# Performance work log

Hardware: AMD Instinct MI355X
Metric: run time of the kernel (lower is better)

## Reference

```python
import jax, jax.numpy as jnp
import numpy as np

B, N, D = 8, 2048, 256

def setup_inputs() -> dict:
    key = jax.random.key(0)
    ks = jax.random.split(key, 8)
    sc = 1.0 / np.sqrt(D)
    return {
        "x": jax.random.normal(ks[0], (B, N, D), dtype=jnp.float32),
        "W_fp": jax.random.normal(ks[1], (D, D), dtype=jnp.float32) * sc,
        "b_fp": jnp.zeros((D,), dtype=jnp.float32),
        "w_s": jax.random.normal(ks[2], (D,), dtype=jnp.float32) * sc,
        "b_s": jnp.zeros((), dtype=jnp.float32),
        "W_rp": jax.random.normal(ks[3], (D, D), dtype=jnp.float32) * sc,
        "b_rp": jnp.zeros((D,), dtype=jnp.float32),
        "W_gp": jax.random.normal(ks[4], (D, D), dtype=jnp.float32) * sc,
        "b_gp": jnp.zeros((D,), dtype=jnp.float32),
        "gamma": jnp.ones((D,), dtype=jnp.float32),
        "beta": jnp.zeros((D,), dtype=jnp.float32),
    }

def reference(x, W_fp, b_fp, w_s, b_s, W_rp, b_rp, W_gp, b_gp, gamma, beta):
    # feature projection: [B, N, D]
    proj = jnp.einsum('bnd,de->bne', x, W_fp) + b_fp
    # F.normalize(p=2, dim=-1) with eps=1e-12
    nrm = jnp.sqrt(jnp.sum(proj * proj, axis=-1, keepdims=True))
    xn = proj / jnp.maximum(nrm, 1e-12)
    # cosine similarity matrix [B, N, N]
    sim = jnp.einsum('bnd,bmd->bnm', xn, xn)
    # adj_scaler: Linear(D,1)+sigmoid is constant along the broadcast axis ->
    # compute per-node scalar once [B, N] (same math as the O(N^2*D) expand)
    s = jax.nn.sigmoid(jnp.einsum('bnd,d->bn', proj, w_s) + b_s)
    scaler = jnp.clip(0.5 * (s[:, :, None] + s[:, None, :]), 1e-6, 1.0)
    adj = jnp.maximum(scaler * sim, 1e-6)  # clamp(min=1e-6)
    degree = jnp.maximum(jnp.sum(adj, axis=2, keepdims=True), 1e-6)
    norm_adj = adj / degree
    # aggregation + region projection
    region = jnp.einsum('bnm,bmd->bnd', norm_adj, proj)
    region = jnp.einsum('bnd,de->bne', region, W_rp) + b_rp
    # global pooling + projection: [B, 1, D]
    g = jnp.mean(region, axis=1, keepdims=True)
    g = jnp.einsum('bnd,de->bne', g, W_gp) + b_gp
    input_global = jnp.mean(x, axis=1, keepdims=True)
    h = g + input_global
    # LayerNorm (eps=1e-5)
    mu = jnp.mean(h, axis=-1, keepdims=True)
    var = jnp.mean((h - mu) ** 2, axis=-1, keepdims=True)
    out = (h - mu) / jnp.sqrt(var + 1e-5) * gamma + beta
    return out, adj
```

## Files before the change

kernel.cpp:

```cpp
#include <hip/hip_runtime.h>
#include <hip/hip_bf16.h>
#include <math.h>

#define Bn 8
#define Nn 2048
#define Dn 256

typedef short short8 __attribute__((ext_vector_type(8)));
typedef float floatx4 __attribute__((ext_vector_type(4)));

__device__ __forceinline__ short f2bf_bits(float f) {
    __bf16 h = (__bf16)f;
    return __builtin_bit_cast(short, h);
}

__device__ __forceinline__ float bf2f(short s) {
    unsigned u = ((unsigned)(unsigned short)s) << 16;
    return __builtin_bit_cast(float, u);
}

__device__ __forceinline__ void gl_lds16(const void* gsrc, void* ldst) {
    __builtin_amdgcn_global_load_lds(
        (const __attribute__((address_space(1))) void*)gsrc,
        (__attribute__((address_space(3))) void*)ldst, 16, 0, 0);
}

__device__ __forceinline__ float sigmoidf_(float z) {
    return 1.0f / (1.0f + __expf(-z));
}



__global__ __launch_bounds__(256) void k_transpose(const float* __restrict__ W,
                                                   short* __restrict__ Wt) {
    __shared__ float Ts[64][65];
    const int t = threadIdx.x;
    const int dt0 = blockIdx.x * 64, et0 = blockIdx.y * 64;
    const int ro = t >> 4, co = (t & 15) * 4;
    #pragma unroll
    for (int rr = 0; rr < 4; ++rr) {
        int row = rr * 16 + ro;
        float4 v = *(const float4*)(W + (size_t)(dt0 + row) * Dn + et0 + co);
        Ts[row][co + 0] = v.x; Ts[row][co + 1] = v.y;
        Ts[row][co + 2] = v.z; Ts[row][co + 3] = v.w;
    }
    __syncthreads();
    const int e = t >> 2, cd0 = (t & 3) * 16;
    short8 a, b;
    #pragma unroll
    for (int i = 0; i < 8; ++i) {
        a[i] = f2bf_bits(Ts[cd0 + i][e]);
        b[i] = f2bf_bits(Ts[cd0 + 8 + i][e]);
    }
    *(short8*)(Wt + (size_t)(et0 + e) * Dn + dt0 + cd0) = a;
    *(short8*)(Wt + (size_t)(et0 + e) * Dn + dt0 + cd0 + 8) = b;
}


__global__ __launch_bounds__(512) void k_projxn(
    const float* __restrict__ x, const short* __restrict__ Wt,
    const float* __restrict__ b_fp, const float* __restrict__ w_s,
    short* __restrict__ xn, float* __restrict__ sdot, float* __restrict__ nrm,
    float* __restrict__ xpart) {
    __shared__ __align__(16) short As[64 * 64];
    __shared__ __align__(16) short Bs[256 * 64];
    __shared__ float xsumS[8 * 256];
    __shared__ float redW[2][64];
    __shared__ float redN[2][64];
    const int t = threadIdx.x;
    const int bm = blockIdx.x * 64;
    const int lane = t & 63, wv = t >> 6;
    const int wm = (wv & 3) * 16;
    const int jh = wv >> 2;
    const int l15 = lane & 15, q = lane >> 4;
    const int rx = l15 & 7;

    for (int i = t; i < 2048; i += 512) xsumS[i] = 0.f;

    floatx4 acc[8];
    #pragma unroll
    for (int j = 0; j < 8; ++j) acc[j] = (floatx4){0.f, 0.f, 0.f, 0.f};

    const int rA = t >> 3, cA = (t & 7) * 8;
    const int rB = t >> 3;
    const int swzA = ((t & 7) ^ (rA & 7)) * 8;
    const int swzBsrc = ((t & 7) ^ (rB & 7)) * 8;
    const int cB = (t & 7) * 8;

    for (int k0 = 0; k0 < Dn; k0 += 64) {
        const float* gp = x + (size_t)(bm + rA) * Dn + k0 + cA;
        float4 v0 = *(const float4*)gp;
        float4 v1 = *(const float4*)(gp + 4);
        short8 o0;
        o0[0] = f2bf_bits(v0.x); o0[1] = f2bf_bits(v0.y);
        o0[2] = f2bf_bits(v0.z); o0[3] = f2bf_bits(v0.w);
        o0[4] = f2bf_bits(v1.x); o0[5] = f2bf_bits(v1.y);
        o0[6] = f2bf_bits(v1.z); o0[7] = f2bf_bits(v1.w);
        *(short8*)(As + rA * 64 + swzA) = o0;
        #pragma unroll
        for (int cc = 0; cc < 4; ++cc)
            gl_lds16(Wt + (size_t)(cc * 64 + rB) * Dn + k0 + swzBsrc,
                     Bs + (cc * 64 + rB) * 64 + cB);
        __syncthreads();
        #pragma unroll
        for (int ks = 0; ks < 2; ++ks) {
            const int cs = ((ks * 4 + q) ^ rx) * 8;
            short8 af = *(const short8*)(As + (wm + l15) * 64 + cs);
            #pragma unroll
            for (int jj = 0; jj < 8; ++jj) {
                short8 bfr = *(const short8*)(Bs + (jh * 128 + jj * 16 + l15) * 64 + cs);
                acc[jj] = __builtin_amdgcn_mfma_f32_16x16x32_bf16(af, bfr, acc[jj], 0, 0, 0);
            }
        }
        {
            float s = 0.f;
            #pragma unroll
            for (int r = 0; r < 8; ++r) {
                int row = wv * 8 + r;
                int idx = ((lane >> 3) ^ (row & 7)) * 8 + (lane & 7);
                s += bf2f(As[row * 64 + idx]);
            }
            xsumS[wv * 256 + k0 + lane] += s;
        }
        __syncthreads();
    }
    if (t < 256) {
        float xs = 0.f;
        #pragma unroll
        for (int w = 0; w < 8; ++w) xs += xsumS[w * 256 + t];
        xpart[(size_t)blockIdx.x * Dn + t] = xs;
    }
    float bfv[8], wsv[8];
    #pragma unroll
    for (int jj = 0; jj < 8; ++jj) {
        bfv[jj] = b_fp[jh * 128 + jj * 16 + l15];
        wsv[jj] = w_s[jh * 128 + jj * 16 + l15];
    }
    float vv[4][8];
    #pragma unroll
    for (int reg = 0; reg < 4; ++reg) {
        float pw = 0.f, pn = 0.f;
        #pragma unroll
        for (int jj = 0; jj < 8; ++jj) {
            float v = acc[jj][reg] + bfv[jj];
            vv[reg][jj] = v;
            pw += v * wsv[jj];
            pn += v * v;
        }
        #pragma unroll
        for (int m = 1; m < 16; m <<= 1) {
            pw += __shfl_xor(pw, m);
            pn += __shfl_xor(pn, m);
        }
        if (l15 == 0) {
            redW[jh][wm + q * 4 + reg] = pw;
            redN[jh][wm + q * 4 + reg] = pn;
        }
    }
    __syncthreads();
    #pragma unroll
    for (int reg = 0; reg < 4; ++reg) {
        int lr = wm + q * 4 + reg;
        float pw = redW[0][lr] + redW[1][lr];
        float pn = redN[0][lr] + redN[1][lr];
        float nc = fmaxf(sqrtf(pn), 1e-12f);
        float inv = 1.0f / nc;
        int row = bm + lr;
        size_t rbase = (size_t)row * Dn + jh * 128 + l15;
        #pragma unroll
        for (int jj = 0; jj < 8; ++jj)
            xn[rbase + jj * 16] = f2bf_bits(vv[reg][jj] * inv);
        if (jh == 0 && l15 == 0) {
            sdot[row] = pw;
            nrm[row] = nc;
        }
    }
}


__global__ __launch_bounds__(512) void k_sim(
    const short* __restrict__ xn, const float* __restrict__ sdot,
    const float* __restrict__ b_s, float* __restrict__ adj,
    float* __restrict__ deg_part) {
    __shared__ __align__(16) short As[128 * 64];
    __shared__ __align__(16) short Bs[256 * 64];
    __shared__ float degS[4][128];
    const int t = threadIdx.x;
    int lin = (blockIdx.z * 16 + blockIdx.y) * 8 + blockIdx.x;
    const int b = lin & 7;
    const int pos = lin >> 3;
    const int by = pos >> 3, cx = pos & 7;
    const int bm = by * 128;
    const int bn = cx * 256;
    const int lane = t & 63, wv = t >> 6;
    const int wm = (wv >> 2) * 64;
    const int wn = (wv & 3) * 64;
    const int l15 = lane & 15, q4 = lane >> 4;
    const int rx = l15 & 7;
    const int rr = t >> 3, c8 = (t & 7) * 8;
    const int swzSrc = ((t & 7) ^ (rr & 7)) * 8;
    const short* xb = xn + (size_t)b * Nn * Dn;

    floatx4 acc[4][4];
    #pragma unroll
    for (int i = 0; i < 4; ++i)
        #pragma unroll
        for (int j = 0; j < 4; ++j) acc[i][j] = (floatx4){0.f, 0.f, 0.f, 0.f};

    for (int k0 = 0; k0 < Dn; k0 += 64) {
        #pragma unroll
        for (int cc = 0; cc < 2; ++cc) {
            int r = cc * 64 + rr;
            gl_lds16(xb + (size_t)(bm + r) * Dn + k0 + swzSrc, As + r * 64 + c8);
        }
        #pragma unroll
        for (int cc = 0; cc < 4; ++cc) {
            int r = cc * 64 + rr;
            gl_lds16(xb + (size_t)(bn + r) * Dn + k0 + swzSrc, Bs + r * 64 + c8);
        }
        __syncthreads();
        #pragma unroll
        for (int ks = 0; ks < 2; ++ks) {
            const int cs = ((ks * 4 + q4) ^ rx) * 8;
            short8 af[4], bfr[4];
            #pragma unroll
            for (int i = 0; i < 4; ++i)
                af[i] = *(const short8*)(As + (wm + i * 16 + l15) * 64 + cs);
            #pragma unroll
            for (int j = 0; j < 4; ++j)
                bfr[j] = *(const short8*)(Bs + (wn + j * 16 + l15) * 64 + cs);
            #pragma unroll
            for (int i = 0; i < 4; ++i)
                #pragma unroll
                for (int j = 0; j < 4; ++j)
                    acc[i][j] = __builtin_amdgcn_mfma_f32_16x16x32_bf16(bfr[j], af[i], acc[i][j], 0, 0, 0);
        }
        __syncthreads();
    }
    const float bsv = b_s[0];
    float srow[4];
    #pragma unroll
    for (int i = 0; i < 4; ++i)
        srow[i] = sigmoidf_(sdot[b * Nn + bm + wm + i * 16 + l15] + bsv);
    float scol[4][4];
    #pragma unroll
    for (int j = 0; j < 4; ++j)
        #pragma unroll
        for (int reg = 0; reg < 4; ++reg)
            scol[j][reg] = sigmoidf_(sdot[b * Nn + bn + wn + j * 16 + q4 * 4 + reg] + bsv);
    #pragma unroll
    for (int i = 0; i < 4; ++i) {
        float rs = 0.f;
        size_t rbase = ((size_t)b * Nn + (bm + wm + i * 16 + l15)) * Nn + bn + wn + q4 * 4;
        #pragma unroll
        for (int j = 0; j < 4; ++j) {
            float4 o;
            float sc;
            sc = fminf(fmaxf(0.5f * (srow[i] + scol[j][0]), 1e-6f), 1.0f);
            o.x = fmaxf(sc * acc[i][j][0], 1e-6f);
            sc = fminf(fmaxf(0.5f * (srow[i] + scol[j][1]), 1e-6f), 1.0f);
            o.y = fmaxf(sc * acc[i][j][1], 1e-6f);
            sc = fminf(fmaxf(0.5f * (srow[i] + scol[j][2]), 1e-6f), 1.0f);
            o.z = fmaxf(sc * acc[i][j][2], 1e-6f);
            sc = fminf(fmaxf(0.5f * (srow[i] + scol[j][3]), 1e-6f), 1.0f);
            o.w = fmaxf(sc * acc[i][j][3], 1e-6f);
            *(float4*)(adj + rbase + (size_t)j * 16) = o;
            rs += o.x + o.y + o.z + o.w;
        }
        rs += __shfl_xor(rs, 16);
        rs += __shfl_xor(rs, 32);
        if (q4 == 0) degS[wv & 3][wm + i * 16 + l15] = rs;
    }
    __syncthreads();
    if (t < 128)
        deg_part[((size_t)(b * 8 + cx)) * Nn + bm + t] =
            degS[0][t] + degS[1][t] + degS[2][t] + degS[3][t];
}


__global__ __launch_bounds__(256) void k_deg(const float* __restrict__ deg_part,
                                             float* __restrict__ invdeg) {
    int b = blockIdx.x, t = blockIdx.y * 256 + threadIdx.x;
    float s = 0.f;
    #pragma unroll
    for (int cx = 0; cx < 8; ++cx)
        s += deg_part[((size_t)(b * 8 + cx)) * Nn + t];
    invdeg[b * Nn + t] = 1.0f / fmaxf(s, 1e-6f);
}


__global__ __launch_bounds__(1024) void k_colsum(
    const float* __restrict__ adj, const float* __restrict__ invdeg,
    const short* __restrict__ xn, const float* __restrict__ nrm,
    float* __restrict__ gpart) {
    int b = blockIdx.x, ck = blockIdx.y, t = threadIdx.x;
    __shared__ float invS[Nn];
    __shared__ float part[64][64];
    __shared__ float csL[64];
    __shared__ float gQ[4][Dn];
    invS[t] = invdeg[b * Nn + t];
    invS[t + 1024] = invdeg[b * Nn + t + 1024];
    __syncthreads();
    const int lc = (t & 15) * 4;
    const int rg = t >> 4;
    const int c0 = ck * 64;
    float sx = 0.f, sy = 0.f, sz = 0.f, sw = 0.f;
    for (int r = rg; r < Nn; r += 64) {
        float4 v = *(const float4*)(adj + ((size_t)b * Nn + r) * Nn + c0 + lc);
        float w = invS[r];
        sx += v.x * w; sy += v.y * w; sz += v.z * w; sw += v.w * w;
    }
    part[rg][lc + 0] = sx; part[rg][lc + 1] = sy;
    part[rg][lc + 2] = sz; part[rg][lc + 3] = sw;
    __syncthreads();
    if (t < 64) {
        float s = 0.f;
        #pragma unroll
        for (int g = 0; g < 64; ++g) s += part[g][t];
        csL[t] = s * nrm[b * Nn + c0 + t];
    }
    __syncthreads();
    {
        int h = t >> 8, d = t & 255;
        float g = 0.f;
        #pragma unroll 4
        for (int mi = 0; mi < 16; ++mi) {
            int m = h * 16 + mi;
            g += csL[m] * bf2f(xn[((size_t)(b * Nn + c0 + m)) * Dn + d]);
        }
        gQ[h][d] = g;
    }
    __syncthreads();
    if (t < Dn)
        gpart[(b * 32 + ck) * Dn + t] = gQ[0][t] + gQ[1][t] + gQ[2][t] + gQ[3][t];
}


__global__ __launch_bounds__(1024) void k_final2(
    const float* __restrict__ gpart, const float* __restrict__ xpart,
    const float* __restrict__ W_rp, const float* __restrict__ b_rp,
    const float* __restrict__ W_gp, const float* __restrict__ b_gp,
    const float* __restrict__ gamma, const float* __restrict__ beta,
    float* __restrict__ out) {
    int b = blockIdx.x, t = threadIdx.x;
    const int d = t & 255, c4 = t >> 8;
    __shared__ float pS[4][Dn];
    __shared__ float xS[4][Dn];
    __shared__ float gp_s[Dn];
    __shared__ float xm_s[Dn];
    __shared__ float g1_s[Dn];
    __shared__ float red[8];
    {
        float gs = 0.f, xs = 0.f;
        #pragma unroll
        for (int k = 0; k < 8; ++k) {
            int ck = c4 * 8 + k;
            gs += gpart[(b * 32 + ck) * Dn + d];
            xs += xpart[(b * 32 + ck) * Dn + d];
        }
        pS[c4][d] = gs;
        xS[c4][d] = xs;
    }
    __syncthreads();
    if (t < Dn) {
        gp_s[t] = (pS[0][t] + pS[1][t] + pS[2][t] + pS[3][t]) * (1.0f / Nn);
        xm_s[t] = (xS[0][t] + xS[1][t] + xS[2][t] + xS[3][t]) * (1.0f / Nn);
    }
    __syncthreads();
    {
        float m1 = 0.f;
        #pragma unroll 4
        for (int i = 0; i < 64; ++i) {
            int dd = c4 * 64 + i;
            m1 += gp_s[dd] * W_rp[dd * Dn + d];
        }
        pS[c4][d] = m1;
    }
    __syncthreads();
    if (t < Dn) g1_s[t] = b_rp[t] + pS[0][t] + pS[1][t] + pS[2][t] + pS[3][t];
    __syncthreads();
    {
        float m2 = 0.f;
        #pragma unroll 4
        for (int i = 0; i < 64; ++i) {
            int ee = c4 * 64 + i;
            m2 += g1_s[ee] * W_gp[ee * Dn + d];
        }
        pS[c4][d] = m2;
    }
    __syncthreads();
    float h = 0.f;
    if (t < Dn) {
        h = b_gp[t] + pS[0][t] + pS[1][t] + pS[2][t] + pS[3][t] + xm_s[t];
        float sum = h;
        #pragma unroll
        for (int m = 1; m < 64; m <<= 1) sum += __shfl_xor(sum, m);
        if ((t & 63) == 0) red[t >> 6] = sum;
    }
    __syncthreads();
    float mu = (red[0] + red[1] + red[2] + red[3]) * (1.0f / Dn);
    if (t < Dn) {
        float dv = h - mu;
        float s2 = dv * dv;
        #pragma unroll
        for (int m = 1; m < 64; m <<= 1) s2 += __shfl_xor(s2, m);
        if ((t & 63) == 0) red[4 + (t >> 6)] = s2;
    }
    __syncthreads();
    if (t < Dn) {
        float dv = h - mu;
        float var = (red[4] + red[5] + red[6] + red[7]) * (1.0f / Dn);
        out[b * Dn + t] = dv * rsqrtf(var + 1e-5f) * gamma[t] + beta[t];
    }
}


extern "C" void kernel_launch(void* const* d_in, const int* in_sizes, int n_in,
                              void* d_out, int out_size, void* d_ws, size_t ws_size,
                              hipStream_t stream) {
    const float* x     = (const float*)d_in[0];
    const float* W_fp  = (const float*)d_in[1];
    const float* b_fp  = (const float*)d_in[2];
    const float* w_s   = (const float*)d_in[3];
    const float* b_s   = (const float*)d_in[4];
    const float* W_rp  = (const float*)d_in[5];
    const float* b_rp  = (const float*)d_in[6];
    const float* W_gp  = (const float*)d_in[7];
    const float* b_gp  = (const float*)d_in[8];
    const float* gamma = (const float*)d_in[9];
    const float* beta  = (const float*)d_in[10];

    float* out = (float*)d_out;
    float* adj = out + Bn * Dn;

    char* ws = (char*)d_ws;
    short* xn     = (short*)(ws);
    short* Wt     = (short*)(ws + 8388608);
    float* sdot   = (float*)(ws + 8519680);
    float* nrm    = (float*)(ws + 8585216);
    float* degp   = (float*)(ws + 8650752);
    float* invdeg = (float*)(ws + 9175040);
    float* gpart  = (float*)(ws + 9699328);
    float* xpart  = (float*)(ws + 9961472);

    k_transpose<<<dim3(4, 4), 256, 0, stream>>>(W_fp, Wt);
    k_projxn<<<(Bn * Nn) / 64, 512, 0, stream>>>(x, Wt, b_fp, w_s, xn, sdot, nrm, xpart);
    k_sim<<<dim3(8, 16, 8), 512, 0, stream>>>(xn, sdot, b_s, adj, degp);
    k_deg<<<dim3(Bn, 8), 256, 0, stream>>>(degp, invdeg);
    k_colsum<<<dim3(Bn, 32), 1024, 0, stream>>>(adj, invdeg, xn, nrm, gpart);
    k_final2<<<Bn, 1024, 0, stream>>>(gpart, xpart, W_rp, b_rp, W_gp, b_gp, gamma, beta, out);
}
```

Before: 237.9 us.

## Fuse degree reduction and final projection into colsum via last-block atomic counter

The separate k_deg kernel is removed: each colsum block now sums the eight degree partials for its batch and computes inverse degrees itself. The k_final2 kernel is folded into k_colsum using a per-batch atomic counter, so the last block to finish a batch runs the pooled projections and LayerNorm. Counters are zeroed in k_transpose. This cuts two kernel launches and their gaps, at the cost of redundant degree reduction in every block (32x per batch) and a serialized tail on the last block.

```diff
diff --git a/kernel.cpp b/kernel.cpp
--- a/kernel.cpp
+++ b/kernel.cpp
@@ -30,11 +30,12 @@
 }
 
 
-
 __global__ __launch_bounds__(256) void k_transpose(const float* __restrict__ W,
-                                                   short* __restrict__ Wt) {
+                                                   short* __restrict__ Wt,
+                                                   unsigned* __restrict__ cnt) {
     __shared__ float Ts[64][65];
     const int t = threadIdx.x;
+    if (blockIdx.x == 0 && blockIdx.y == 0 && t < 8) cnt[t] = 0u;
     const int dt0 = blockIdx.x * 64, et0 = blockIdx.y * 64;
     const int ro = t >> 4, co = (t & 15) * 4;
     #pragma unroll
@@ -278,28 +279,29 @@
 }
 
 
-__global__ __launch_bounds__(256) void k_deg(const float* __restrict__ deg_part,
-                                             float* __restrict__ invdeg) {
-    int b = blockIdx.x, t = blockIdx.y * 256 + threadIdx.x;
-    float s = 0.f;
-    #pragma unroll
-    for (int cx = 0; cx < 8; ++cx)
-        s += deg_part[((size_t)(b * 8 + cx)) * Nn + t];
-    invdeg[b * Nn + t] = 1.0f / fmaxf(s, 1e-6f);
-}
-
-
 __global__ __launch_bounds__(1024) void k_colsum(
-    const float* __restrict__ adj, const float* __restrict__ invdeg,
+    const float* __restrict__ adj, const float* __restrict__ deg_part,
     const short* __restrict__ xn, const float* __restrict__ nrm,
-    float* __restrict__ gpart) {
+    float* __restrict__ gpart, const float* __restrict__ xpart,
+    const float* __restrict__ W_rp, const float* __restrict__ b_rp,
+    const float* __restrict__ W_gp, const float* __restrict__ b_gp,
+    const float* __restrict__ gamma, const float* __restrict__ beta,
+    float* __restrict__ out, unsigned* __restrict__ cnt) {
     int b = blockIdx.x, ck = blockIdx.y, t = threadIdx.x;
     __shared__ float invS[Nn];
     __shared__ float part[64][64];
     __shared__ float csL[64];
     __shared__ float gQ[4][Dn];
-    invS[t] = invdeg[b * Nn + t];
-    invS[t + 1024] = invdeg[b * Nn + t + 1024];
+    __shared__ int doneFlag;
+    #pragma unroll
+    for (int rc = 0; rc < 2; ++rc) {
+        int row = rc * 1024 + t;
+        float s = 0.f;
+        #pragma unroll
+        for (int cx = 0; cx < 8; ++cx)
+            s += deg_part[((size_t)(b * 8 + cx)) * Nn + row];
+        invS[row] = 1.0f / fmaxf(s, 1e-6f);
+    }
     __syncthreads();
     const int lc = (t & 15) * 4;
     const int rg = t >> 4;
@@ -333,84 +335,85 @@
     __syncthreads();
     if (t < Dn)
         gpart[(b * 32 + ck) * Dn + t] = gQ[0][t] + gQ[1][t] + gQ[2][t] + gQ[3][t];
-}
-
-
-__global__ __launch_bounds__(1024) void k_final2(
-    const float* __restrict__ gpart, const float* __restrict__ xpart,
-    const float* __restrict__ W_rp, const float* __restrict__ b_rp,
-    const float* __restrict__ W_gp, const float* __restrict__ b_gp,
-    const float* __restrict__ gamma, const float* __restrict__ beta,
-    float* __restrict__ out) {
-    int b = blockIdx.x, t = threadIdx.x;
-    const int d = t & 255, c4 = t >> 8;
-    __shared__ float pS[4][Dn];
-    __shared__ float xS[4][Dn];
-    __shared__ float gp_s[Dn];
-    __shared__ float xm_s[Dn];
-    __shared__ float g1_s[Dn];
-    __shared__ float red[8];
+    __syncthreads();
+    if (t == 0) {
+        __threadfence();
+        unsigned old = atomicAdd(&cnt[b], 1u);
+        doneFlag = (old == 31u);
+    }
+    __syncthreads();
+    if (!doneFlag) return;
+    __threadfence();
     {
-        float gs = 0.f, xs = 0.f;
-        #pragma unroll
-        for (int k = 0; k < 8; ++k) {
-            int ck = c4 * 8 + k;
-            gs += gpart[(b * 32 + ck) * Dn + d];
-            xs += xpart[(b * 32 + ck) * Dn + d];
-        }
-        pS[c4][d] = gs;
-        xS[c4][d] = xs;
-    }
-    __syncthreads();
-    if (t < Dn) {
-        gp_s[t] = (pS[0][t] + pS[1][t] + pS[2][t] + pS[3][t]) * (1.0f / Nn);
-        xm_s[t] = (xS[0][t] + xS[1][t] + xS[2][t] + xS[3][t]) * (1.0f / Nn);
-    }
-    __syncthreads();
-    {
-        float m1 = 0.f;
-        #pragma unroll 4
-        for (int i = 0; i < 64; ++i) {
-            int dd = c4 * 64 + i;
-            m1 += gp_s[dd] * W_rp[dd * Dn + d];
-        }
-        pS[c4][d] = m1;
-    }
-    __syncthreads();
-    if (t < Dn) g1_s[t] = b_rp[t] + pS[0][t] + pS[1][t] + pS[2][t] + pS[3][t];
-    __syncthreads();
-    {
-        float m2 = 0.f;
-        #pragma unroll 4
-        for (int i = 0; i < 64; ++i) {
-            int ee = c4 * 64 + i;
-            m2 += g1_s[ee] * W_gp[ee * Dn + d];
-        }
-        pS[c4][d] = m2;
-    }
-    __syncthreads();
-    float h = 0.f;
-    if (t < Dn) {
-        h = b_gp[t] + pS[0][t] + pS[1][t] + pS[2][t] + pS[3][t] + xm_s[t];
-        float sum = h;
-        #pragma unroll
-        for (int m = 1; m < 64; m <<= 1) sum += __shfl_xor(sum, m);
-        if ((t & 63) == 0) red[t >> 6] = sum;
-    }
-    __syncthreads();
-    float mu = (red[0] + red[1] + red[2] + red[3]) * (1.0f / Dn);
-    if (t < Dn) {
-        float dv = h - mu;
-        float s2 = dv * dv;
-        #pragma unroll
-        for (int m = 1; m < 64; m <<= 1) s2 += __shfl_xor(s2, m);
-        if ((t & 63) == 0) red[4 + (t >> 6)] = s2;
-    }
-    __syncthreads();
-    if (t < Dn) {
-        float dv = h - mu;
-        float var = (red[4] + red[5] + red[6] + red[7]) * (1.0f / Dn);
-        out[b * Dn + t] = dv * rsqrtf(var + 1e-5f) * gamma[t] + beta[t];
+        const int d = t & 255, c4 = t >> 8;
+        float (*pS)[Dn] = (float(*)[Dn])&part[0][0];
+        float (*xS)[Dn] = (float(*)[Dn])&part[16][0];
+        float* gp_s = &part[32][0];
+        float* xm_s = &part[36][0];
+        float* g1_s = &part[40][0];
+        float* red  = &part[44][0];
+        {
+            float gs = 0.f, xs = 0.f;
+            #pragma unroll
+            for (int k = 0; k < 8; ++k) {
+                int kk = c4 * 8 + k;
+                gs += gpart[(b * 32 + kk) * Dn + d];
+                xs += xpart[(b * 32 + kk) * Dn + d];
+            }
+            pS[c4][d] = gs;
+            xS[c4][d] = xs;
+        }
+        __syncthreads();
+        if (t < Dn) {
+            gp_s[t] = (pS[0][t] + pS[1][t] + pS[2][t] + pS[3][t]) * (1.0f / Nn);
+            xm_s[t] = (xS[0][t] + xS[1][t] + xS[2][t] + xS[3][t]) * (1.0f / Nn);
+        }
+        __syncthreads();
+        {
+            float m1 = 0.f;
+            #pragma unroll 4
+            for (int i = 0; i < 64; ++i) {
+                int dd = c4 * 64 + i;
+                m1 += gp_s[dd] * W_rp[dd * Dn + d];
+            }
+            pS[c4][d] = m1;
+        }
+        __syncthreads();
+        if (t < Dn) g1_s[t] = b_rp[t] + pS[0][t] + pS[1][t] + pS[2][t] + pS[3][t];
+        __syncthreads();
+        {
+            float m2 = 0.f;
+            #pragma unroll 4
+            for (int i = 0; i < 64; ++i) {
+                int ee = c4 * 64 + i;
+                m2 += g1_s[ee] * W_gp[ee * Dn + d];
+            }
+            pS[c4][d] = m2;
+        }
+        __syncthreads();
+        float h = 0.f;
+        if (t < Dn) {
+            h = b_gp[t] + pS[0][t] + pS[1][t] + pS[2][t] + pS[3][t] + xm_s[t];
+            float sum = h;
+            #pragma unroll
+            for (int m = 1; m < 64; m <<= 1) sum += __shfl_xor(sum, m);
+            if ((t & 63) == 0) red[t >> 6] = sum;
+        }
+        __syncthreads();
+        float mu = (red[0] + red[1] + red[2] + red[3]) * (1.0f / Dn);
+        if (t < Dn) {
+            float dv = h - mu;
+            float s2 = dv * dv;
+            #pragma unroll
+            for (int m = 1; m < 64; m <<= 1) s2 += __shfl_xor(s2, m);
+            if ((t & 63) == 0) red[4 + (t >> 6)] = s2;
+        }
+        __syncthreads();
+        if (t < Dn) {
+            float dv = h - mu;
+            float var = (red[4] + red[5] + red[6] + red[7]) * (1.0f / Dn);
+            out[b * Dn + t] = dv * rsqrtf(var + 1e-5f) * gamma[t] + beta[t];
+        }
     }
 }
 
@@ -434,19 +437,19 @@
     float* adj = out + Bn * Dn;
 
     char* ws = (char*)d_ws;
-    short* xn     = (short*)(ws);
-    short* Wt     = (short*)(ws + 8388608);
-    float* sdot   = (float*)(ws + 8519680);
-    float* nrm    = (float*)(ws + 8585216);
-    float* degp   = (float*)(ws + 8650752);
-    float* invdeg = (float*)(ws + 9175040);
-    float* gpart  = (float*)(ws + 9699328);
-    float* xpart  = (float*)(ws + 9961472);
-
-    k_transpose<<<dim3(4, 4), 256, 0, stream>>>(W_fp, Wt);
+    short* xn      = (short*)(ws);
+    short* Wt      = (short*)(ws + 8388608);
+    float* sdot    = (float*)(ws + 8519680);
+    float* nrm     = (float*)(ws + 8585216);
+    float* degp    = (float*)(ws + 8650752);
+    unsigned* cnt  = (unsigned*)(ws + 9240576);
+    float* gpart   = (float*)(ws + 9699328);
+    float* xpart   = (float*)(ws + 9961472);
+
+    k_transpose<<<dim3(4, 4), 256, 0, stream>>>(W_fp, Wt, cnt);
     k_projxn<<<(Bn * Nn) / 64, 512, 0, stream>>>(x, Wt, b_fp, w_s, xn, sdot, nrm, xpart);
     k_sim<<<dim3(8, 16, 8), 512, 0, stream>>>(xn, sdot, b_s, adj, degp);
-    k_deg<<<dim3(Bn, 8), 256, 0, stream>>>(degp, invdeg);
-    k_colsum<<<dim3(Bn, 32), 1024, 0, stream>>>(adj, invdeg, xn, nrm, gpart);
-    k_final2<<<Bn, 1024, 0, stream>>>(gpart, xpart, W_rp, b_rp, W_gp, b_gp, gamma, beta, out);
-}
+    k_colsum<<<dim3(Bn, 32), 1024, 0, stream>>>(adj, degp, xn, nrm, gpart, xpart,
+                                                W_rp, b_rp, W_gp, b_gp,
+                                                gamma, beta, out, cnt);
+}
```

After: 244.4 us. +2.8%, slower.
